# Performance work log

Hardware: AMD Instinct MI355X
Metric: run time of the kernel (lower is better)

Reference implementation:

```python
import jax, jax.numpy as jnp
import numpy as np

N, E, H, FN, FE = 50000, 800000, 128, 8, 4


def setup_inputs() -> dict:
    key = jax.random.key(0)
    ks = jax.random.split(key, 12)
    g = lambda k, shape: jax.random.normal(k, shape, dtype=jnp.float32) * 0.05
    return dict(
        x=jax.random.normal(ks[0], (N, FN), dtype=jnp.float32),
        edge_index=jax.random.randint(ks[1], (2, E), 0, N),
        edge_attr=jax.random.normal(ks[2], (E, FE), dtype=jnp.float32),
        W1=g(ks[3], (FN, H)), b1=jnp.zeros((H,), jnp.float32),
        W2=g(ks[4], (H, H)), b2=jnp.zeros((H,), jnp.float32),
        W3=g(ks[5], (H, H)), b3=jnp.zeros((H,), jnp.float32),
        We1=g(ks[6], (FE, H)), be1=jnp.zeros((H,), jnp.float32),
        We2=g(ks[7], (H, H)), be2=jnp.zeros((H,), jnp.float32),
        Wc1=g(ks[8], (3 * H, H)), bc1=jnp.zeros((H,), jnp.float32),
        Wc2=g(ks[9], (H, H // 2)), bc2=jnp.zeros((H // 2,), jnp.float32),
        Wc3=g(ks[10], (H // 2, 2)), bc3=jnp.zeros((2,), jnp.float32),
    )


def _gcn(h, W, b, row2, col2, norm, n):
    # GCNConv: transform, normalized message from source row2 -> target col2, scatter-add, bias
    h = h @ W
    msg = norm[:, None] * h[row2]  # [E+N, H]
    return jax.ops.segment_sum(msg, col2, num_segments=n) + b


def reference(x, edge_index, edge_attr, W1, b1, W2, b2, W3, b3,
              We1, be1, We2, be2, Wc1, bc1, Wc2, bc2, Wc3, bc3):
    n = x.shape[0]
    row, col = edge_index[0], edge_index[1]
    loop = jnp.arange(n)
    # add self-loops (PyG GCNConv default)
    row2 = jnp.concatenate([row, loop])
    col2 = jnp.concatenate([col, loop])
    deg = jax.ops.segment_sum(jnp.ones_like(col2, dtype=x.dtype), col2, num_segments=n)
    dinv = jnp.where(deg > 0, deg ** -0.5, 0.0)
    norm = dinv[row2] * dinv[col2]  # symmetric normalization per edge

    h = jax.nn.relu(_gcn(x, W1, b1, row2, col2, norm, n))
    h = jax.nn.relu(_gcn(h, W2, b2, row2, col2, norm, n))
    h = jax.nn.relu(_gcn(h, W3, b3, row2, col2, norm, n))

    # edge encoder MLP (dropout inactive in eval)
    ef = jax.nn.relu(edge_attr @ We1 + be1) @ We2 + be2

    # gather endpoint node features, concat with edge features
    ec = jnp.concatenate([h[row], h[col], ef], axis=1)  # [E, 3H]
    z = jax.nn.relu(ec @ Wc1 + bc1)
    z = jax.nn.relu(z @ Wc2 + bc2)
    logits = z @ Wc3 + bc3
    return jax.nn.log_softmax(logits, axis=1)
```

## Files before the change

### kernel.cpp

```cpp
#include <hip/hip_runtime.h>
#include <math.h>

#define H 128
#define STC 152
#define SOT 136
#define SPQ 136
#define Z2S 69

typedef __attribute__((ext_vector_type(8))) short short8;
typedef __attribute__((ext_vector_type(4))) float f32x4;

__device__ inline unsigned short f2bf(float f) {
    unsigned int u = __float_as_uint(f);
    return (unsigned short)((u + 0x7fffu + ((u >> 16) & 1u)) >> 16);
}
__device__ inline float bflo(unsigned int v) { return __uint_as_float(v << 16); }
__device__ inline float bfhi(unsigned int v) { return __uint_as_float(v & 0xffff0000u); }
__device__ inline float bf2f(unsigned short v) { return __uint_as_float(((unsigned int)v) << 16); }

__device__ inline void fma4(float4& acc, float a, const float4 w) {
    acc.x = fmaf(a, w.x, acc.x);
    acc.y = fmaf(a, w.y, acc.y);
    acc.z = fmaf(a, w.z, acc.z);
    acc.w = fmaf(a, w.w, acc.w);
}


__global__ void count_kernel(const int* __restrict__ col, int E, int* __restrict__ cnt) {
    int e = blockIdx.x * blockDim.x + threadIdx.x;
    if (e < E) atomicAdd(&cnt[col[e]], 1);
}

__global__ void scan_sum_kernel(const int* __restrict__ cnt, int N, int* __restrict__ bsum) {
    int b = blockIdx.x, t = threadIdx.x;
    int base = b * 1024 + t * 4;
    int s = 0;
#pragma unroll
    for (int g = 0; g < 4; ++g) {
        int i = base + g;
        if (i < N) s += cnt[i];
    }
    for (int off = 32; off >= 1; off >>= 1) s += __shfl_down(s, off, 64);
    __shared__ int ws[4];
    if ((t & 63) == 0) ws[t >> 6] = s;
    __syncthreads();
    if (t == 0) bsum[b] = ws[0] + ws[1] + ws[2] + ws[3];
}

__global__ void scan_offsets_kernel(const int* __restrict__ bsum, int nb,
                                    int* __restrict__ boff, int* __restrict__ col_start, int N) {
    int lane = threadIdx.x;
    int v = (lane < nb) ? bsum[lane] : 0;
    int incl = v;
    for (int off = 1; off < 64; off <<= 1) {
        int u = __shfl_up(incl, off, 64);
        if (lane >= off) incl += u;
    }
    if (lane < nb) boff[lane] = incl - v;
    if (lane == 63) col_start[N] = incl;
}

__global__ void scan_write_kernel(const int* __restrict__ cnt, int N, const int* __restrict__ boff,
                                  int* __restrict__ col_start, int* __restrict__ cursor,
                                  float* __restrict__ dinv) {
    int b = blockIdx.x, t = threadIdx.x;
    int lane = t & 63, wv = t >> 6;
    int base = b * 1024 + t * 4;
    int c[4];
    int s = 0;
#pragma unroll
    for (int g = 0; g < 4; ++g) {
        int i = base + g;
        c[g] = (i < N) ? cnt[i] : 0;
        s += c[g];
    }
    int incl = s;
    for (int off = 1; off < 64; off <<= 1) {
        int u = __shfl_up(incl, off, 64);
        if (lane >= off) incl += u;
    }
    __shared__ int ws[4];
    if (lane == 63) ws[wv] = incl;
    __syncthreads();
    int run = boff[b] + incl - s;
    for (int w = 0; w < wv; ++w) run += ws[w];
#pragma unroll
    for (int g = 0; g < 4; ++g) {
        int i = base + g;
        if (i < N) {
            col_start[i] = run;
            cursor[i] = run;
            dinv[i] = rsqrtf((float)(c[g] + 1));
            run += c[g];
        }
    }
}

__global__ void scatter_kernel(const int* __restrict__ row, const int* __restrict__ col, int E,
                               int* __restrict__ cursor, int* __restrict__ csc_src,
                               int2* __restrict__ csc_ec) {
    int e = blockIdx.x * blockDim.x + threadIdx.x;
    if (e < E) {
        int c = col[e];
        int p = atomicAdd(&cursor[c], 1);
        csc_src[p] = row[e];
        csc_ec[p] = make_int2(e, c);
    }
}


__global__ __launch_bounds__(256) void aggx_kernel(
    const float* __restrict__ x, const int* __restrict__ col_start,
    const int* __restrict__ csc_src, const float* __restrict__ dinv,
    float* __restrict__ aggx, int N) {
    int wv = threadIdx.x >> 6, lane = threadIdx.x & 63;
    int i = blockIdx.x * 4 + wv;
    if (i >= N) return;
    int f = lane & 7, j = lane >> 3;
    int s0 = col_start[i], s1 = col_start[i + 1];
    float acc = 0.f;
    int p = s0 + j;
    for (; p + 8 < s1; p += 16) {
        int sa = csc_src[p], sb = csc_src[p + 8];
        float va = dinv[sa] * x[sa * 8 + f];
        float vb = dinv[sb] * x[sb * 8 + f];
        acc += va + vb;
    }
    if (p < s1) {
        int s = csc_src[p];
        acc = fmaf(dinv[s], x[s * 8 + f], acc);
    }
    acc += __shfl_xor(acc, 8, 64);
    acc += __shfl_xor(acc, 16, 64);
    acc += __shfl_xor(acc, 32, 64);
    if (j == 0) {
        float di = dinv[i];
        aggx[i * 8 + f] = fmaf(di, acc, di * di * x[i * 8 + f]);
    }
}

__global__ void xform8bf_kernel(const float* __restrict__ aggx, const float* __restrict__ W,
                                const float* __restrict__ b, const float* __restrict__ dinv,
                                unsigned int* __restrict__ out, int N) {
    int t = blockIdx.x * 256 + threadIdx.x;
    int i = t >> 6, jp = t & 63;
    if (i >= N) return;
    const float* ar = aggx + i * 8;
    float sc = dinv[i];
    int j0 = jp * 2;
    float a0 = b[j0], a1 = b[j0 + 1];
#pragma unroll
    for (int k = 0; k < 8; ++k) {
        float av = ar[k];
        a0 = fmaf(av, W[k * 128 + j0], a0);
        a1 = fmaf(av, W[k * 128 + j0 + 1], a1);
    }
    out[(size_t)i * 64 + jp] = (unsigned int)f2bf(sc * fmaxf(a0, 0.f)) |
                               ((unsigned int)f2bf(sc * fmaxf(a1, 0.f)) << 16);
}

__global__ __launch_bounds__(256) void agg128bf_kernel(
    const unsigned int* __restrict__ hd, const int* __restrict__ col_start,
    const int* __restrict__ csc_src, const float* __restrict__ dinv,
    unsigned int* __restrict__ out, int N) {
    int wv = threadIdx.x >> 6, lane = threadIdx.x & 63;
    int i = blockIdx.x * 4 + wv;
    if (i >= N) return;
    int s0 = col_start[i], s1 = col_start[i + 1];
    float ax = 0.f, ay = 0.f;
    int p = s0;
    for (; p + 16 <= s1; p += 16) {
        unsigned int v[16];
#pragma unroll
        for (int k = 0; k < 16; ++k)
            v[k] = hd[(size_t)csc_src[p + k] * 64 + lane];
#pragma unroll
        for (int k = 0; k < 16; ++k) { ax += bflo(v[k]); ay += bfhi(v[k]); }
    }
    for (; p + 4 <= s1; p += 4) {
        unsigned int v0 = hd[(size_t)csc_src[p + 0] * 64 + lane];
        unsigned int v1 = hd[(size_t)csc_src[p + 1] * 64 + lane];
        unsigned int v2 = hd[(size_t)csc_src[p + 2] * 64 + lane];
        unsigned int v3 = hd[(size_t)csc_src[p + 3] * 64 + lane];
        ax += bflo(v0) + bflo(v1) + bflo(v2) + bflo(v3);
        ay += bfhi(v0) + bfhi(v1) + bfhi(v2) + bfhi(v3);
    }
    for (; p < s1; ++p) {
        unsigned int v = hd[(size_t)csc_src[p] * 64 + lane];
        ax += bflo(v); ay += bfhi(v);
    }
    float di = dinv[i];
    unsigned int vs = hd[(size_t)i * 64 + lane];
    float rx = di * (ax + bflo(vs));
    float ry = di * (ay + bfhi(vs));
    out[(size_t)i * 64 + lane] = (unsigned int)f2bf(rx) | ((unsigned int)f2bf(ry) << 16);
}

__global__ __launch_bounds__(256) void xform_mfma_kernel(
    const unsigned short* __restrict__ in, const unsigned short* __restrict__ Bp,
    const float* __restrict__ b, const float* __restrict__ scale,
    unsigned short* __restrict__ out, int N) {
    __shared__ __align__(16) unsigned short sm[64 * STC];
    int tid = threadIdx.x;
    int i0 = blockIdx.x * 64;
    for (int u = tid; u < 1024; u += 256) {
        int i = u >> 4, l = u & 15;
        int node = i0 + i; if (node >= N) node = N - 1;
        uint4 v = ((const uint4*)in)[(size_t)node * 16 + l];
        *(uint4*)&sm[i * STC + l * 8] = v;
    }
    __syncthreads();
    int lane = tid & 63, w = tid >> 6, lm = lane & 15, quad = lane >> 4;
    int nt0 = 2 * w, nt1 = 2 * w + 1;
    f32x4 acc0[4], acc1[4];
    {
        float bv0 = b[nt0 * 16 + lm], bv1 = b[nt1 * 16 + lm];
        for (int m = 0; m < 4; ++m)
            for (int r = 0; r < 4; ++r) { acc0[m][r] = bv0; acc1[m][r] = bv1; }
    }
#pragma unroll
    for (int s = 0; s < 4; ++s) {
        short8 b0 = *(const short8*)&Bp[((size_t)(s * 8 + nt0) * 64 + lane) * 8];
        short8 b1 = *(const short8*)&Bp[((size_t)(s * 8 + nt1) * 64 + lane) * 8];
#pragma unroll
        for (int m = 0; m < 4; ++m) {
            short8 afr = *(const short8*)&sm[(m * 16 + lm) * STC + s * 32 + quad * 8];
            acc0[m] = __builtin_amdgcn_mfma_f32_16x16x32_bf16(afr, b0, acc0[m], 0, 0, 0);
            acc1[m] = __builtin_amdgcn_mfma_f32_16x16x32_bf16(afr, b1, acc1[m], 0, 0, 0);
        }
    }
    __syncthreads();
    for (int m = 0; m < 4; ++m)
        for (int r = 0; r < 4; ++r) {
            int rw = m * 16 + quad * 4 + r;
            int node = i0 + rw; if (node >= N) node = N - 1;
            float sc = scale ? scale[node] : 1.f;
            sm[rw * SOT + nt0 * 16 + lm] = f2bf(sc * fmaxf(acc0[m][r], 0.f));
            sm[rw * SOT + nt1 * 16 + lm] = f2bf(sc * fmaxf(acc1[m][r], 0.f));
        }
    __syncthreads();
    for (int u = tid; u < 1024; u += 256) {
        int i = u >> 4, l = u & 15;
        int node = i0 + i;
        if (node < N)
            *(uint4*)&out[(size_t)node * 128 + l * 8] = *(uint4*)&sm[i * SOT + l * 8];
    }
}


__global__ void weff_kernel(const float* __restrict__ We2, const float* __restrict__ Wc1,
                            float* __restrict__ Weff) {
    int idx = blockIdx.x * blockDim.x + threadIdx.x;
    int k = idx >> 7, c = idx & 127;
    float acc = 0.f;
    for (int j = 0; j < 128; ++j)
        acc = fmaf(We2[k * 128 + j], Wc1[(256 + j) * 128 + c], acc);
    Weff[idx] = acc;
}

__global__ void bc1p_kernel(const float* __restrict__ bc1, const float* __restrict__ be2,
                            const float* __restrict__ Wc1, float* __restrict__ bc1p) {
    int c = threadIdx.x;
    float acc = bc1[c];
    for (int j = 0; j < 128; ++j)
        acc = fmaf(be2[j], Wc1[(256 + j) * 128 + c], acc);
    bc1p[c] = acc;
}

__global__ void packg_kernel(const float* __restrict__ src, unsigned short* __restrict__ dst) {
    int idx = blockIdx.x * 256 + threadIdx.x;
    int s = idx >> 9, nt = (idx >> 6) & 7, lane = idx & 63;
    int quad = lane >> 4, lm = lane & 15;
    int n = nt * 16 + lm, k0 = s * 32 + quad * 8;
    unsigned int p[4];
#pragma unroll
    for (int g = 0; g < 4; ++g) {
        p[g] = (unsigned int)f2bf(src[(k0 + 2 * g) * 128 + n]) |
               ((unsigned int)f2bf(src[(k0 + 2 * g + 1) * 128 + n]) << 16);
    }
    *(uint4*)&dst[(size_t)idx * 8] = make_uint4(p[0], p[1], p[2], p[3]);
}

__global__ void pack2_kernel(const float* __restrict__ Wc2, unsigned short* __restrict__ Bp2) {
    int idx = blockIdx.x * 256 + threadIdx.x;
    int s = idx >> 8, nt = (idx >> 6) & 3, lane = idx & 63;
    int quad = lane >> 4, lm = lane & 15;
    int n = nt * 16 + lm, k0 = s * 32 + quad * 8;
    unsigned int p[4];
#pragma unroll
    for (int g = 0; g < 4; ++g) {
        p[g] = (unsigned int)f2bf(Wc2[(k0 + 2 * g) * 64 + n]) |
               ((unsigned int)f2bf(Wc2[(k0 + 2 * g + 1) * 64 + n]) << 16);
    }
    *(uint4*)&Bp2[(size_t)idx * 8] = make_uint4(p[0], p[1], p[2], p[3]);
}

__global__ void packwe1_kernel(const float* __restrict__ We1, const float* __restrict__ be1,
                               unsigned short* __restrict__ BpE) {
    int idx = blockIdx.x * 256 + threadIdx.x;
    if (idx >= 512) return;
    int nt = idx >> 6, lane = idx & 63;
    int quad = lane >> 4, lm = lane & 15;
    int n = nt * 16 + lm, k0 = quad * 8;
    unsigned int p[4];
#pragma unroll
    for (int g = 0; g < 4; ++g) {
        int r0 = k0 + 2 * g, r1 = r0 + 1;
        float v0 = (r0 < 4) ? We1[r0 * 128 + n] : ((r0 == 4) ? be1[n] : 0.f);
        float v1 = (r1 < 4) ? We1[r1 * 128 + n] : ((r1 == 4) ? be1[n] : 0.f);
        p[g] = (unsigned int)f2bf(v0) | ((unsigned int)f2bf(v1) << 16);
    }
    *(uint4*)&BpE[(size_t)idx * 8] = make_uint4(p[0], p[1], p[2], p[3]);
}


__global__ __launch_bounds__(256) void h3pq_kernel(
    const unsigned short* __restrict__ in, const unsigned short* __restrict__ BpW3,
    const float* __restrict__ b3,
    const unsigned short* __restrict__ BpA, const unsigned short* __restrict__ BpB,
    const float* __restrict__ bc1p,
    unsigned short* __restrict__ P, unsigned short* __restrict__ Q, int N) {
    __shared__ __align__(16) unsigned short At[64 * STC];
    __shared__ __align__(16) unsigned short Hs[64 * SOT];
    int tid = threadIdx.x;
    int i0 = blockIdx.x * 64;
    for (int u = tid; u < 1024; u += 256) {
        int i = u >> 4, l = u & 15;
        int node = i0 + i; if (node >= N) node = N - 1;
        uint4 v = ((const uint4*)in)[(size_t)node * 16 + l];
        *(uint4*)&At[i * STC + l * 8] = v;
    }
    __syncthreads();
    int lane = tid & 63, w = tid >> 6, lm = lane & 15, quad = lane >> 4;

    {
        int nt0 = 2 * w, nt1 = 2 * w + 1;
        f32x4 a0[4], a1[4];
        float bv0 = b3[nt0 * 16 + lm], bv1 = b3[nt1 * 16 + lm];
        for (int m = 0; m < 4; ++m)
            for (int r = 0; r < 4; ++r) { a0[m][r] = bv0; a1[m][r] = bv1; }
#pragma unroll
        for (int s = 0; s < 4; ++s) {
            short8 b0 = *(const short8*)&BpW3[((size_t)(s * 8 + nt0) * 64 + lane) * 8];
            short8 b1 = *(const short8*)&BpW3[((size_t)(s * 8 + nt1) * 64 + lane) * 8];
#pragma unroll
            for (int m = 0; m < 4; ++m) {
                short8 afr = *(const short8*)&At[(m * 16 + lm) * STC + s * 32 + quad * 8];
                a0[m] = __builtin_amdgcn_mfma_f32_16x16x32_bf16(afr, b0, a0[m], 0, 0, 0);
                a1[m] = __builtin_amdgcn_mfma_f32_16x16x32_bf16(afr, b1, a1[m], 0, 0, 0);
            }
        }
        __syncthreads();
        for (int m = 0; m < 4; ++m)
            for (int r = 0; r < 4; ++r) {
                int rw = m * 16 + quad * 4 + r;
                Hs[rw * SOT + nt0 * 16 + lm] = f2bf(fmaxf(a0[m][r], 0.f));
                Hs[rw * SOT + nt1 * 16 + lm] = f2bf(fmaxf(a1[m][r], 0.f));
            }
    }
    __syncthreads();

    int half = w & 1;
    const unsigned short* Bp = (w >> 1) ? BpB : BpA;
    f32x4 acc[4][4];
    for (int nt = 0; nt < 4; ++nt) {
        float bv = (w >> 1) ? 0.f : bc1p[half * 64 + nt * 16 + lm];
        for (int m = 0; m < 4; ++m)
            for (int r = 0; r < 4; ++r) acc[nt][m][r] = bv;
    }
#pragma unroll
    for (int s = 0; s < 4; ++s) {
        short8 afr[4];
#pragma unroll
        for (int m = 0; m < 4; ++m)
            afr[m] = *(const short8*)&Hs[(m * 16 + lm) * SOT + s * 32 + quad * 8];
#pragma unroll
        for (int nt = 0; nt < 4; ++nt) {
            short8 bfr = *(const short8*)&Bp[((size_t)(s * 8 + half * 4 + nt) * 64 + lane) * 8];
#pragma unroll
            for (int m = 0; m < 4; ++m)
                acc[nt][m] = __builtin_amdgcn_mfma_f32_16x16x32_bf16(afr[m], bfr, acc[nt][m], 0, 0, 0);
        }
    }
    __syncthreads();
    unsigned short* St = At;

    if (w < 2) {
        for (int nt = 0; nt < 4; ++nt)
            for (int m = 0; m < 4; ++m)
                for (int r = 0; r < 4; ++r) {
                    int rw = m * 16 + quad * 4 + r;
                    St[rw * SOT + half * 64 + nt * 16 + lm] = f2bf(acc[nt][m][r]);
                }
    }
    __syncthreads();
    for (int u = tid; u < 1024; u += 256) {
        int i = u >> 4, l = u & 15;
        int node = i0 + i;
        if (node < N)
            *(uint4*)&P[(size_t)node * 128 + l * 8] = *(uint4*)&St[i * SOT + l * 8];
    }
    __syncthreads();
    if (w >= 2) {
        for (int nt = 0; nt < 4; ++nt)
            for (int m = 0; m < 4; ++m)
                for (int r = 0; r < 4; ++r) {
                    int rw = m * 16 + quad * 4 + r;
                    St[rw * SOT + half * 64 + nt * 16 + lm] = f2bf(acc[nt][m][r]);
                }
    }
    __syncthreads();
    for (int u = tid; u < 1024; u += 256) {
        int i = u >> 4, l = u & 15;
        int node = i0 + i;
        if (node < N)
            *(uint4*)&Q[(size_t)node * 128 + l * 8] = *(uint4*)&St[i * SOT + l * 8];
    }
}


__global__ __launch_bounds__(256, 4) void classifier_mfma2(
    const int* __restrict__ csc_src, const int2* __restrict__ csc_ec,
    const float* __restrict__ ea, const unsigned short* __restrict__ BpE,
    const unsigned short* __restrict__ P, const unsigned short* __restrict__ Q,
    const unsigned short* __restrict__ BpU, const unsigned short* __restrict__ Bp2,
    const float* __restrict__ bc2, const float* __restrict__ Wc3, const float* __restrict__ bc3,
    float* __restrict__ out, int E) {
    __shared__ __align__(16) unsigned char smem[37888];
    unsigned short* SpqB = (unsigned short*)smem;
    float* z2 = (float*)smem;
    unsigned short* At = (unsigned short*)(smem + 17664);
    unsigned short* z1 = At;
    float* part = (float*)(smem + 17664);
    int* sS = (int*)(smem + 37120);
    int* eS = sS + 64;
    int* cS = eS + 64;

    int tid = threadIdx.x;
    int lane = tid & 63, w = tid >> 6, lm = lane & 15, quad = lane >> 4;
    int e0 = blockIdx.x * 64;

    short8 bE0 = *(const short8*)&BpE[((size_t)(2 * w) * 64 + lane) * 8];
    short8 bE1 = *(const short8*)&BpE[((size_t)(2 * w + 1) * 64 + lane) * 8];
    short8 b0s[4], b1s[4], b2s[4];
#pragma unroll
    for (int s = 0; s < 4; ++s) {
        b0s[s] = *(const short8*)&BpU[((size_t)(s * 8 + 2 * w) * 64 + lane) * 8];
        b1s[s] = *(const short8*)&BpU[((size_t)(s * 8 + 2 * w + 1) * 64 + lane) * 8];
        b2s[s] = *(const short8*)&Bp2[((size_t)(s * 4 + w) * 64 + lane) * 8];
    }
    float bv2 = bc2[w * 16 + lm];

    if (tid < 64) {
        int p = e0 + tid; if (p >= E) p = E - 1;
        sS[tid] = csc_src[p];
        int2 ec = csc_ec[p];
        eS[tid] = ec.x; cS[tid] = ec.y;
    }
    __syncthreads();

    {
        const uint4* P4 = (const uint4*)P;
        const uint4* Q4 = (const uint4*)Q;
        int l = tid & 15;
#pragma unroll
        for (int j = 0; j < 4; ++j) {
            int i = (tid >> 4) + 16 * j;
            uint4 pv = P4[(size_t)sS[i] * 16 + l];
            uint4 qv = Q4[(size_t)cS[i] * 16 + l];
            unsigned int o0 = (unsigned int)f2bf(bflo(pv.x) + bflo(qv.x)) |
                              ((unsigned int)f2bf(bfhi(pv.x) + bfhi(qv.x)) << 16);
            unsigned int o1 = (unsigned int)f2bf(bflo(pv.y) + bflo(qv.y)) |
                              ((unsigned int)f2bf(bfhi(pv.y) + bfhi(qv.y)) << 16);
            unsigned int o2 = (unsigned int)f2bf(bflo(pv.z) + bflo(qv.z)) |
                              ((unsigned int)f2bf(bfhi(pv.z) + bfhi(qv.z)) << 16);
            unsigned int o3 = (unsigned int)f2bf(bflo(pv.w) + bflo(qv.w)) |
                              ((unsigned int)f2bf(bfhi(pv.w) + bfhi(qv.w)) << 16);
            *(uint4*)&SpqB[i * SPQ + l * 8] = make_uint4(o0, o1, o2, o3);
        }
    }

    short8 eaf[4];
#pragma unroll
    for (int m = 0; m < 4; ++m) eaf[m] = (short8){0, 0, 0, 0, 0, 0, 0, 0};
    if (quad == 0) {
#pragma unroll
        for (int m = 0; m < 4; ++m) {
            int ed = eS[m * 16 + lm];
            float4 a = ((const float4*)ea)[ed];
            eaf[m][0] = (short)f2bf(a.x);
            eaf[m][1] = (short)f2bf(a.y);
            eaf[m][2] = (short)f2bf(a.z);
            eaf[m][3] = (short)f2bf(a.w);
            eaf[m][4] = (short)0x3F80;
        }
    }

    {
        f32x4 zacc = {0.f, 0.f, 0.f, 0.f};
#pragma unroll
        for (int m = 0; m < 4; ++m) {
            f32x4 t0 = __builtin_amdgcn_mfma_f32_16x16x32_bf16(eaf[m], bE0, zacc, 0, 0, 0);
            f32x4 t1 = __builtin_amdgcn_mfma_f32_16x16x32_bf16(eaf[m], bE1, zacc, 0, 0, 0);
#pragma unroll
            for (int r = 0; r < 4; ++r) {
                int rw = m * 16 + quad * 4 + r;
                At[rw * STC + 32 * w + lm]      = f2bf(fmaxf(t0[r], 0.f));
                At[rw * STC + 32 * w + 16 + lm] = f2bf(fmaxf(t1[r], 0.f));
            }
        }
    }
    __syncthreads();

    f32x4 acc0[4], acc1[4];
    for (int m = 0; m < 4; ++m)
        for (int r = 0; r < 4; ++r) { acc0[m][r] = 0.f; acc1[m][r] = 0.f; }
#pragma unroll
    for (int s = 0; s < 4; ++s) {
#pragma unroll
        for (int m = 0; m < 4; ++m) {
            short8 afr = *(const short8*)&At[(m * 16 + lm) * STC + s * 32 + quad * 8];
            acc0[m] = __builtin_amdgcn_mfma_f32_16x16x32_bf16(afr, b0s[s], acc0[m], 0, 0, 0);
            acc1[m] = __builtin_amdgcn_mfma_f32_16x16x32_bf16(afr, b1s[s], acc1[m], 0, 0, 0);
        }
    }
    for (int m = 0; m < 4; ++m)
        for (int r = 0; r < 4; ++r) {
            int rw = m * 16 + quad * 4 + r;
            acc0[m][r] = fmaxf(acc0[m][r] + bf2f(SpqB[rw * SPQ + 32 * w + lm]), 0.f);
            acc1[m][r] = fmaxf(acc1[m][r] + bf2f(SpqB[rw * SPQ + 32 * w + 16 + lm]), 0.f);
        }
    __syncthreads();
    for (int m = 0; m < 4; ++m)
        for (int r = 0; r < 4; ++r) {
            int rw = m * 16 + quad * 4 + r;
            z1[rw * STC + 32 * w + lm]      = f2bf(acc0[m][r]);
            z1[rw * STC + 32 * w + 16 + lm] = f2bf(acc1[m][r]);
        }
    __syncthreads();

    {
        f32x4 acc2[4];
        for (int m = 0; m < 4; ++m)
            for (int r = 0; r < 4; ++r) acc2[m][r] = bv2;
#pragma unroll
        for (int s = 0; s < 4; ++s) {
#pragma unroll
            for (int m = 0; m < 4; ++m) {
                short8 afr = *(const short8*)&z1[(m * 16 + lm) * STC + s * 32 + quad * 8];
                acc2[m] = __builtin_amdgcn_mfma_f32_16x16x32_bf16(afr, b2s[s], acc2[m], 0, 0, 0);
            }
        }
        for (int m = 0; m < 4; ++m)
            for (int r = 0; r < 4; ++r)
                z2[(m * 16 + quad * 4 + r) * Z2S + w * 16 + lm] = fmaxf(acc2[m][r], 0.f);
    }
    __syncthreads();

    {
        int e = tid & 63, q = tid >> 6;
        int c = q & 1, hf = q >> 1;
        const float* zr = z2 + e * Z2S + hf * 32;
        const float* wc = Wc3 + hf * 64 + c;
        float acc = 0.f;
#pragma unroll 8
        for (int kk = 0; kk < 32; ++kk)
            acc = fmaf(zr[kk], wc[2 * kk], acc);
        part[q * 64 + e] = acc;
    }
    __syncthreads();
    if (tid < 64) {
        int p = e0 + tid;
        if (p < E) {
            float l0 = bc3[0] + part[tid] + part[128 + tid];
            float l1 = bc3[1] + part[64 + tid] + part[192 + tid];
            float m = fmaxf(l0, l1);
            float lse = m + logf(expf(l0 - m) + expf(l1 - m));
            ((float2*)out)[eS[tid]] = make_float2(l0 - lse, l1 - lse);
        }
    }
}


extern "C" void kernel_launch(void* const* d_in, const int* in_sizes, int n_in,
                              void* d_out, int out_size, void* d_ws, size_t ws_size,
                              hipStream_t stream) {
    const float* x   = (const float*)d_in[0];
    const int*   ei  = (const int*)d_in[1];
    const float* ea  = (const float*)d_in[2];
    const float* W1  = (const float*)d_in[3];
    const float* b1  = (const float*)d_in[4];
    const float* W2  = (const float*)d_in[5];
    const float* b2  = (const float*)d_in[6];
    const float* W3  = (const float*)d_in[7];
    const float* b3  = (const float*)d_in[8];
    const float* We1 = (const float*)d_in[9];
    const float* be1 = (const float*)d_in[10];
    const float* We2 = (const float*)d_in[11];
    const float* be2 = (const float*)d_in[12];
    const float* Wc1 = (const float*)d_in[13];
    const float* bc1 = (const float*)d_in[14];
    const float* Wc2 = (const float*)d_in[15];
    const float* bc2 = (const float*)d_in[16];
    const float* Wc3 = (const float*)d_in[17];
    const float* bc3 = (const float*)d_in[18];
    float* out = (float*)d_out;

    int N = in_sizes[0] / 8;
    int E = in_sizes[1] / 2;
    const int* row = ei;
    const int* col = ei + E;
    int NB = (N + 1023) / 1024;
    int ntiles = (E + 63) / 64;

    char* w = (char*)d_ws;
    auto alloc = [&](size_t bytes) { void* p = (void*)w; w += (bytes + 255) & ~(size_t)255; return p; };
    int*   cnt       = (int*)alloc((size_t)N * 4);
    int*   col_start = (int*)alloc((size_t)(N + 1) * 4);
    int*   cursor    = (int*)alloc((size_t)N * 4);
    int*   csc_src   = (int*)alloc((size_t)E * 4);
    int2*  csc_ec    = (int2*)alloc((size_t)E * 8);
    float* dinv      = (float*)alloc((size_t)N * 4);
    int*   bsum      = (int*)alloc(64 * 4);
    int*   boff      = (int*)alloc(64 * 4);
    float* Weff      = (float*)alloc(128 * 128 * 4);
    float* bc1p      = (float*)alloc(128 * 4);
    unsigned short* BpA  = (unsigned short*)alloc(32768);
    unsigned short* BpB  = (unsigned short*)alloc(32768);
    unsigned short* BpU  = (unsigned short*)alloc(32768);
    unsigned short* BpW2 = (unsigned short*)alloc(32768);
    unsigned short* BpW3 = (unsigned short*)alloc(32768);
    unsigned short* Bp2  = (unsigned short*)alloc(16384);
    unsigned short* BpE  = (unsigned short*)alloc(8192);
    float* aggx = (float*)alloc((size_t)N * 8 * 4);
    unsigned short* bufA = (unsigned short*)alloc((size_t)N * H * 2);
    unsigned short* bufB = (unsigned short*)alloc((size_t)N * H * 2);
    unsigned short* Pm   = (unsigned short*)alloc((size_t)N * H * 2);
    unsigned short* Qm   = (unsigned short*)alloc((size_t)N * H * 2);

    hipMemsetAsync(cnt, 0, (size_t)N * 4, stream);
    count_kernel<<<(E + 255) / 256, 256, 0, stream>>>(col, E, cnt);
    scan_sum_kernel<<<NB, 256, 0, stream>>>(cnt, N, bsum);
    scan_offsets_kernel<<<1, 64, 0, stream>>>(bsum, NB, boff, col_start, N);
    scan_write_kernel<<<NB, 256, 0, stream>>>(cnt, N, boff, col_start, cursor, dinv);
    scatter_kernel<<<(E + 255) / 256, 256, 0, stream>>>(row, col, E, cursor, csc_src, csc_ec);

    weff_kernel<<<64, 256, 0, stream>>>(We2, Wc1, Weff);
    bc1p_kernel<<<1, 128, 0, stream>>>(bc1, be2, Wc1, bc1p);
    packg_kernel<<<8, 256, 0, stream>>>(Wc1, BpA);
    packg_kernel<<<8, 256, 0, stream>>>(Wc1 + 128 * 128, BpB);
    packg_kernel<<<8, 256, 0, stream>>>(Weff, BpU);
    packg_kernel<<<8, 256, 0, stream>>>(W2, BpW2);
    packg_kernel<<<8, 256, 0, stream>>>(W3, BpW3);
    pack2_kernel<<<4, 256, 0, stream>>>(Wc2, Bp2);
    packwe1_kernel<<<2, 256, 0, stream>>>(We1, be1, BpE);

    aggx_kernel<<<(N + 3) / 4, 256, 0, stream>>>(x, col_start, csc_src, dinv, aggx, N);
    xform8bf_kernel<<<(N * 64 + 255) / 256, 256, 0, stream>>>(aggx, W1, b1, dinv,
                                                              (unsigned int*)bufA, N);
    agg128bf_kernel<<<(N + 3) / 4, 256, 0, stream>>>((const unsigned int*)bufA, col_start, csc_src,
                                                     dinv, (unsigned int*)bufB, N);
    xform_mfma_kernel<<<(N + 63) / 64, 256, 0, stream>>>(bufB, BpW2, b2, dinv, bufA, N);
    agg128bf_kernel<<<(N + 3) / 4, 256, 0, stream>>>((const unsigned int*)bufA, col_start, csc_src,
                                                     dinv, (unsigned int*)bufB, N);
    h3pq_kernel<<<(N + 63) / 64, 256, 0, stream>>>(bufB, BpW3, b3, BpA, BpB, bc1p, Pm, Qm, N);

    classifier_mfma2<<<ntiles, 256, 0, stream>>>(
        csc_src, csc_ec, ea, BpE, Pm, Qm, BpU, Bp2, bc2, Wc3, bc3, out, E);
}
```

Baseline: 462.4 us.

## Fuse GCN aggregation with per-layer transforms and merge weight-packing launches

```diff
diff --git a/kernel.cpp b/kernel.cpp
--- a/kernel.cpp
+++ b/kernel.cpp
@@ -109,145 +109,6 @@
 }
 
 
-__global__ __launch_bounds__(256) void aggx_kernel(
-    const float* __restrict__ x, const int* __restrict__ col_start,
-    const int* __restrict__ csc_src, const float* __restrict__ dinv,
-    float* __restrict__ aggx, int N) {
-    int wv = threadIdx.x >> 6, lane = threadIdx.x & 63;
-    int i = blockIdx.x * 4 + wv;
-    if (i >= N) return;
-    int f = lane & 7, j = lane >> 3;
-    int s0 = col_start[i], s1 = col_start[i + 1];
-    float acc = 0.f;
-    int p = s0 + j;
-    for (; p + 8 < s1; p += 16) {
-        int sa = csc_src[p], sb = csc_src[p + 8];
-        float va = dinv[sa] * x[sa * 8 + f];
-        float vb = dinv[sb] * x[sb * 8 + f];
-        acc += va + vb;
-    }
-    if (p < s1) {
-        int s = csc_src[p];
-        acc = fmaf(dinv[s], x[s * 8 + f], acc);
-    }
-    acc += __shfl_xor(acc, 8, 64);
-    acc += __shfl_xor(acc, 16, 64);
-    acc += __shfl_xor(acc, 32, 64);
-    if (j == 0) {
-        float di = dinv[i];
-        aggx[i * 8 + f] = fmaf(di, acc, di * di * x[i * 8 + f]);
-    }
-}
-
-__global__ void xform8bf_kernel(const float* __restrict__ aggx, const float* __restrict__ W,
-                                const float* __restrict__ b, const float* __restrict__ dinv,
-                                unsigned int* __restrict__ out, int N) {
-    int t = blockIdx.x * 256 + threadIdx.x;
-    int i = t >> 6, jp = t & 63;
-    if (i >= N) return;
-    const float* ar = aggx + i * 8;
-    float sc = dinv[i];
-    int j0 = jp * 2;
-    float a0 = b[j0], a1 = b[j0 + 1];
-#pragma unroll
-    for (int k = 0; k < 8; ++k) {
-        float av = ar[k];
-        a0 = fmaf(av, W[k * 128 + j0], a0);
-        a1 = fmaf(av, W[k * 128 + j0 + 1], a1);
-    }
-    out[(size_t)i * 64 + jp] = (unsigned int)f2bf(sc * fmaxf(a0, 0.f)) |
-                               ((unsigned int)f2bf(sc * fmaxf(a1, 0.f)) << 16);
-}
-
-__global__ __launch_bounds__(256) void agg128bf_kernel(
-    const unsigned int* __restrict__ hd, const int* __restrict__ col_start,
-    const int* __restrict__ csc_src, const float* __restrict__ dinv,
-    unsigned int* __restrict__ out, int N) {
-    int wv = threadIdx.x >> 6, lane = threadIdx.x & 63;
-    int i = blockIdx.x * 4 + wv;
-    if (i >= N) return;
-    int s0 = col_start[i], s1 = col_start[i + 1];
-    float ax = 0.f, ay = 0.f;
-    int p = s0;
-    for (; p + 16 <= s1; p += 16) {
-        unsigned int v[16];
-#pragma unroll
-        for (int k = 0; k < 16; ++k)
-            v[k] = hd[(size_t)csc_src[p + k] * 64 + lane];
-#pragma unroll
-        for (int k = 0; k < 16; ++k) { ax += bflo(v[k]); ay += bfhi(v[k]); }
-    }
-    for (; p + 4 <= s1; p += 4) {
-        unsigned int v0 = hd[(size_t)csc_src[p + 0] * 64 + lane];
-        unsigned int v1 = hd[(size_t)csc_src[p + 1] * 64 + lane];
-        unsigned int v2 = hd[(size_t)csc_src[p + 2] * 64 + lane];
-        unsigned int v3 = hd[(size_t)csc_src[p + 3] * 64 + lane];
-        ax += bflo(v0) + bflo(v1) + bflo(v2) + bflo(v3);
-        ay += bfhi(v0) + bfhi(v1) + bfhi(v2) + bfhi(v3);
-    }
-    for (; p < s1; ++p) {
-        unsigned int v = hd[(size_t)csc_src[p] * 64 + lane];
-        ax += bflo(v); ay += bfhi(v);
-    }
-    float di = dinv[i];
-    unsigned int vs = hd[(size_t)i * 64 + lane];
-    float rx = di * (ax + bflo(vs));
-    float ry = di * (ay + bfhi(vs));
-    out[(size_t)i * 64 + lane] = (unsigned int)f2bf(rx) | ((unsigned int)f2bf(ry) << 16);
-}
-
-__global__ __launch_bounds__(256) void xform_mfma_kernel(
-    const unsigned short* __restrict__ in, const unsigned short* __restrict__ Bp,
-    const float* __restrict__ b, const float* __restrict__ scale,
-    unsigned short* __restrict__ out, int N) {
-    __shared__ __align__(16) unsigned short sm[64 * STC];
-    int tid = threadIdx.x;
-    int i0 = blockIdx.x * 64;
-    for (int u = tid; u < 1024; u += 256) {
-        int i = u >> 4, l = u & 15;
-        int node = i0 + i; if (node >= N) node = N - 1;
-        uint4 v = ((const uint4*)in)[(size_t)node * 16 + l];
-        *(uint4*)&sm[i * STC + l * 8] = v;
-    }
-    __syncthreads();
-    int lane = tid & 63, w = tid >> 6, lm = lane & 15, quad = lane >> 4;
-    int nt0 = 2 * w, nt1 = 2 * w + 1;
-    f32x4 acc0[4], acc1[4];
-    {
-        float bv0 = b[nt0 * 16 + lm], bv1 = b[nt1 * 16 + lm];
-        for (int m = 0; m < 4; ++m)
-            for (int r = 0; r < 4; ++r) { acc0[m][r] = bv0; acc1[m][r] = bv1; }
-    }
-#pragma unroll
-    for (int s = 0; s < 4; ++s) {
-        short8 b0 = *(const short8*)&Bp[((size_t)(s * 8 + nt0) * 64 + lane) * 8];
-        short8 b1 = *(const short8*)&Bp[((size_t)(s * 8 + nt1) * 64 + lane) * 8];
-#pragma unroll
-        for (int m = 0; m < 4; ++m) {
-            short8 afr = *(const short8*)&sm[(m * 16 + lm) * STC + s * 32 + quad * 8];
-            acc0[m] = __builtin_amdgcn_mfma_f32_16x16x32_bf16(afr, b0, acc0[m], 0, 0, 0);
-            acc1[m] = __builtin_amdgcn_mfma_f32_16x16x32_bf16(afr, b1, acc1[m], 0, 0, 0);
-        }
-    }
-    __syncthreads();
-    for (int m = 0; m < 4; ++m)
-        for (int r = 0; r < 4; ++r) {
-            int rw = m * 16 + quad * 4 + r;
-            int node = i0 + rw; if (node >= N) node = N - 1;
-            float sc = scale ? scale[node] : 1.f;
-            sm[rw * SOT + nt0 * 16 + lm] = f2bf(sc * fmaxf(acc0[m][r], 0.f));
-            sm[rw * SOT + nt1 * 16 + lm] = f2bf(sc * fmaxf(acc1[m][r], 0.f));
-        }
-    __syncthreads();
-    for (int u = tid; u < 1024; u += 256) {
-        int i = u >> 4, l = u & 15;
-        int node = i0 + i;
-        if (node < N)
-            *(uint4*)&out[(size_t)node * 128 + l * 8] = *(uint4*)&sm[i * SOT + l * 8];
-    }
-}
-
-
 __global__ void weff_kernel(const float* __restrict__ We2, const float* __restrict__ Wc1,
                             float* __restrict__ Weff) {
     int idx = blockIdx.x * blockDim.x + threadIdx.x;
@@ -267,150 +128,320 @@
     bc1p[c] = acc;
 }
 
-__global__ void packg_kernel(const float* __restrict__ src, unsigned short* __restrict__ dst) {
-    int idx = blockIdx.x * 256 + threadIdx.x;
-    int s = idx >> 9, nt = (idx >> 6) & 7, lane = idx & 63;
-    int quad = lane >> 4, lm = lane & 15;
-    int n = nt * 16 + lm, k0 = s * 32 + quad * 8;
-    unsigned int p[4];
-#pragma unroll
-    for (int g = 0; g < 4; ++g) {
-        p[g] = (unsigned int)f2bf(src[(k0 + 2 * g) * 128 + n]) |
-               ((unsigned int)f2bf(src[(k0 + 2 * g + 1) * 128 + n]) << 16);
-    }
-    *(uint4*)&dst[(size_t)idx * 8] = make_uint4(p[0], p[1], p[2], p[3]);
-}
-
-__global__ void pack2_kernel(const float* __restrict__ Wc2, unsigned short* __restrict__ Bp2) {
-    int idx = blockIdx.x * 256 + threadIdx.x;
-    int s = idx >> 8, nt = (idx >> 6) & 3, lane = idx & 63;
-    int quad = lane >> 4, lm = lane & 15;
-    int n = nt * 16 + lm, k0 = s * 32 + quad * 8;
-    unsigned int p[4];
-#pragma unroll
-    for (int g = 0; g < 4; ++g) {
-        p[g] = (unsigned int)f2bf(Wc2[(k0 + 2 * g) * 64 + n]) |
-               ((unsigned int)f2bf(Wc2[(k0 + 2 * g + 1) * 64 + n]) << 16);
-    }
-    *(uint4*)&Bp2[(size_t)idx * 8] = make_uint4(p[0], p[1], p[2], p[3]);
-}
-
-__global__ void packwe1_kernel(const float* __restrict__ We1, const float* __restrict__ be1,
-                               unsigned short* __restrict__ BpE) {
-    int idx = blockIdx.x * 256 + threadIdx.x;
-    if (idx >= 512) return;
-    int nt = idx >> 6, lane = idx & 63;
-    int quad = lane >> 4, lm = lane & 15;
-    int n = nt * 16 + lm, k0 = quad * 8;
-    unsigned int p[4];
-#pragma unroll
-    for (int g = 0; g < 4; ++g) {
-        int r0 = k0 + 2 * g, r1 = r0 + 1;
-        float v0 = (r0 < 4) ? We1[r0 * 128 + n] : ((r0 == 4) ? be1[n] : 0.f);
-        float v1 = (r1 < 4) ? We1[r1 * 128 + n] : ((r1 == 4) ? be1[n] : 0.f);
-        p[g] = (unsigned int)f2bf(v0) | ((unsigned int)f2bf(v1) << 16);
-    }
-    *(uint4*)&BpE[(size_t)idx * 8] = make_uint4(p[0], p[1], p[2], p[3]);
-}
-
-
-__global__ __launch_bounds__(256) void h3pq_kernel(
-    const unsigned short* __restrict__ in, const unsigned short* __restrict__ BpW3,
-    const float* __restrict__ b3,
+__global__ void pack_all_kernel(const float* __restrict__ Wc1, const float* __restrict__ Weff,
+                                const float* __restrict__ W2, const float* __restrict__ W3,
+                                const float* __restrict__ Wc2,
+                                const float* __restrict__ We1, const float* __restrict__ be1,
+                                unsigned short* __restrict__ BpA, unsigned short* __restrict__ BpB,
+                                unsigned short* __restrict__ BpU, unsigned short* __restrict__ BpW2,
+                                unsigned short* __restrict__ BpW3, unsigned short* __restrict__ Bp2,
+                                unsigned short* __restrict__ BpE) {
+    int b = blockIdx.x;
+    if (b < 40) {
+        const float* src;
+        unsigned short* dst;
+        int which = b >> 3;
+        if (which == 0)      { src = Wc1;          dst = BpA; }
+        else if (which == 1) { src = Wc1 + 16384;  dst = BpB; }
+        else if (which == 2) { src = Weff;         dst = BpU; }
+        else if (which == 3) { src = W2;           dst = BpW2; }
+        else                 { src = W3;           dst = BpW3; }
+        int idx = (b & 7) * 256 + threadIdx.x;
+        int s = idx >> 9, nt = (idx >> 6) & 7, lane = idx & 63;
+        int quad = lane >> 4, lm = lane & 15;
+        int n = nt * 16 + lm, k0 = s * 32 + quad * 8;
+        unsigned int p[4];
+#pragma unroll
+        for (int g = 0; g < 4; ++g) {
+            p[g] = (unsigned int)f2bf(src[(k0 + 2 * g) * 128 + n]) |
+                   ((unsigned int)f2bf(src[(k0 + 2 * g + 1) * 128 + n]) << 16);
+        }
+        *(uint4*)&dst[(size_t)idx * 8] = make_uint4(p[0], p[1], p[2], p[3]);
+    } else if (b < 44) {
+        int idx = (b - 40) * 256 + threadIdx.x;
+        int s = idx >> 8, nt = (idx >> 6) & 3, lane = idx & 63;
+        int quad = lane >> 4, lm = lane & 15;
+        int n = nt * 16 + lm, k0 = s * 32 + quad * 8;
+        unsigned int p[4];
+#pragma unroll
+        for (int g = 0; g < 4; ++g) {
+            p[g] = (unsigned int)f2bf(Wc2[(k0 + 2 * g) * 64 + n]) |
+                   ((unsigned int)f2bf(Wc2[(k0 + 2 * g + 1) * 64 + n]) << 16);
+        }
+        *(uint4*)&Bp2[(size_t)idx * 8] = make_uint4(p[0], p[1], p[2], p[3]);
+    } else {
+        int idx = (b - 44) * 256 + threadIdx.x;
+        if (idx < 512) {
+            int nt = idx >> 6, lane = idx & 63;
+            int quad = lane >> 4, lm = lane & 15;
+            int n = nt * 16 + lm, k0 = quad * 8;
+            unsigned int p[4];
+#pragma unroll
+            for (int g = 0; g < 4; ++g) {
+                int r0 = k0 + 2 * g, r1 = r0 + 1;
+                float v0 = (r0 < 4) ? We1[r0 * 128 + n] : ((r0 == 4) ? be1[n] : 0.f);
+                float v1 = (r1 < 4) ? We1[r1 * 128 + n] : ((r1 == 4) ? be1[n] : 0.f);
+                p[g] = (unsigned int)f2bf(v0) | ((unsigned int)f2bf(v1) << 16);
+            }
+            *(uint4*)&BpE[(size_t)idx * 8] = make_uint4(p[0], p[1], p[2], p[3]);
+        }
+    }
+}
+
+
+__global__ __launch_bounds__(256) void layer1_kernel(
+    const float* __restrict__ x, const int* __restrict__ col_start,
+    const int* __restrict__ csc_src, const float* __restrict__ dinv,
+    const float* __restrict__ W1, const float* __restrict__ b1,
+    unsigned int* __restrict__ out, int N) {
+    __shared__ float ax_s[64][8];
+    int tid = threadIdx.x, wv = tid >> 6, lane = tid & 63;
+    int i0 = blockIdx.x * 64;
+    int f = lane & 7, j = lane >> 3;
+    for (int k = 0; k < 16; ++k) {
+        int i = i0 + wv * 16 + k;
+        if (i < N) {
+            int s0 = col_start[i], s1 = col_start[i + 1];
+            float acc = 0.f;
+            int p = s0 + j;
+            for (; p + 8 < s1; p += 16) {
+                int sa = csc_src[p], sb = csc_src[p + 8];
+                acc += dinv[sa] * x[sa * 8 + f] + dinv[sb] * x[sb * 8 + f];
+            }
+            if (p < s1) {
+                int s = csc_src[p];
+                acc = fmaf(dinv[s], x[s * 8 + f], acc);
+            }
+            acc += __shfl_xor(acc, 8, 64);
+            acc += __shfl_xor(acc, 16, 64);
+            acc += __shfl_xor(acc, 32, 64);
+            if (j == 0) {
+                float di = dinv[i];
+                ax_s[wv * 16 + k][f] = fmaf(di, acc, di * di * x[i * 8 + f]);
+            }
+        }
+    }
+    __syncthreads();
+    for (int u = tid; u < 4096; u += 256) {
+        int k = u >> 6, jp = u & 63;
+        int node = i0 + k;
+        if (node >= N) continue;
+        const float* ar = ax_s[k];
+        float sc = dinv[node];
+        int j0 = jp * 2;
+        float a0 = b1[j0], a1 = b1[j0 + 1];
+#pragma unroll
+        for (int kk = 0; kk < 8; ++kk) {
+            float av = ar[kk];
+            a0 = fmaf(av, W1[kk * 128 + j0], a0);
+            a1 = fmaf(av, W1[kk * 128 + j0 + 1], a1);
+        }
+        out[(size_t)node * 64 + jp] = (unsigned int)f2bf(sc * fmaxf(a0, 0.f)) |
+                                      ((unsigned int)f2bf(sc * fmaxf(a1, 0.f)) << 16);
+    }
+}
+
+__global__ __launch_bounds__(512) void layer2_kernel(
+    const unsigned int* __restrict__ hd, const int* __restrict__ col_start,
+    const int* __restrict__ csc_src, const float* __restrict__ dinv,
+    const unsigned short* __restrict__ Bp, const float* __restrict__ b,
+    const float* __restrict__ scale, unsigned short* __restrict__ out, int N) {
+    __shared__ __align__(16) unsigned short At[64 * STC];
+    int tid = threadIdx.x, wv = tid >> 6, lane = tid & 63;
+    int lm = lane & 15, quad = lane >> 4;
+    int i0 = blockIdx.x * 64;
+
+    short8 bs[4];
+#pragma unroll
+    for (int s = 0; s < 4; ++s)
+        bs[s] = *(const short8*)&Bp[((size_t)(s * 8 + wv) * 64 + lane) * 8];
+    float bv = b[wv * 16 + lm];
+
+    unsigned int* At32 = (unsigned int*)At;
+    for (int k = 0; k < 8; ++k) {
+        int i = i0 + wv * 8 + k;
+        int ii = (i < N) ? i : N - 1;
+        int s0 = col_start[ii], s1 = col_start[ii + 1];
+        float ax = 0.f, ay = 0.f;
+        int p = s0;
+        for (; p + 16 <= s1; p += 16) {
+            unsigned int v[16];
+#pragma unroll
+            for (int t = 0; t < 16; ++t) v[t] = hd[(size_t)csc_src[p + t] * 64 + lane];
+#pragma unroll
+            for (int t = 0; t < 16; ++t) { ax += bflo(v[t]); ay += bfhi(v[t]); }
+        }
+        for (; p + 4 <= s1; p += 4) {
+            unsigned int v0 = hd[(size_t)csc_src[p + 0] * 64 + lane];
+            unsigned int v1 = hd[(size_t)csc_src[p + 1] * 64 + lane];
+            unsigned int v2 = hd[(size_t)csc_src[p + 2] * 64 + lane];
+            unsigned int v3 = hd[(size_t)csc_src[p + 3] * 64 + lane];
+            ax += bflo(v0) + bflo(v1) + bflo(v2) + bflo(v3);
+            ay += bfhi(v0) + bfhi(v1) + bfhi(v2) + bfhi(v3);
+        }
+        for (; p < s1; ++p) {
+            unsigned int v = hd[(size_t)csc_src[p] * 64 + lane];
+            ax += bflo(v); ay += bfhi(v);
+        }
+        float di = dinv[ii];
+        unsigned int vs = hd[(size_t)ii * 64 + lane];
+        float rx = di * (ax + bflo(vs));
+        float ry = di * (ay + bfhi(vs));
+        At32[(wv * 8 + k) * 76 + lane] = (unsigned int)f2bf(rx) | ((unsigned int)f2bf(ry) << 16);
+    }
+    __syncthreads();
+
+    f32x4 acc[4];
+    for (int m = 0; m < 4; ++m)
+        for (int r = 0; r < 4; ++r) acc[m][r] = bv;
+#pragma unroll
+    for (int s = 0; s < 4; ++s) {
+#pragma unroll
+        for (int m = 0; m < 4; ++m) {
+            short8 afr = *(const short8*)&At[(m * 16 + lm) * STC + s * 32 + quad * 8];
+            acc[m] = __builtin_amdgcn_mfma_f32_16x16x32_bf16(afr, bs[s], acc[m], 0, 0, 0);
+        }
+    }
+    __syncthreads();
+    for (int m = 0; m < 4; ++m)
+        for (int r = 0; r < 4; ++r) {
+            int rw = m * 16 + quad * 4 + r;
+            int node = i0 + rw; if (node >= N) node = N - 1;
+            float sc = scale ? scale[node] : 1.f;
+            At[rw * SOT + wv * 16 + lm] = f2bf(sc * fmaxf(acc[m][r], 0.f));
+        }
+    __syncthreads();
+    for (int u = tid; u < 1024; u += 512) {
+        int i = u >> 4, l = u & 15;
+        int node = i0 + i;
+        if (node < N)
+            *(uint4*)&out[(size_t)node * 128 + l * 8] = *(uint4*)&At[i * SOT + l * 8];
+    }
+}
+
+__global__ __launch_bounds__(512) void layer3_kernel(
+    const unsigned int* __restrict__ hd, const int* __restrict__ col_start,
+    const int* __restrict__ csc_src, const float* __restrict__ dinv,
+    const unsigned short* __restrict__ BpW3, const float* __restrict__ b3,
     const unsigned short* __restrict__ BpA, const unsigned short* __restrict__ BpB,
     const float* __restrict__ bc1p,
     unsigned short* __restrict__ P, unsigned short* __restrict__ Q, int N) {
     __shared__ __align__(16) unsigned short At[64 * STC];
     __shared__ __align__(16) unsigned short Hs[64 * SOT];
-    int tid = threadIdx.x;
+    int tid = threadIdx.x, wv = tid >> 6, lane = tid & 63;
+    int lm = lane & 15, quad = lane >> 4;
     int i0 = blockIdx.x * 64;
-    for (int u = tid; u < 1024; u += 256) {
-        int i = u >> 4, l = u & 15;
-        int node = i0 + i; if (node >= N) node = N - 1;
-        uint4 v = ((const uint4*)in)[(size_t)node * 16 + l];
-        *(uint4*)&At[i * STC + l * 8] = v;
-    }
-    __syncthreads();
-    int lane = tid & 63, w = tid >> 6, lm = lane & 15, quad = lane >> 4;
+
+    short8 bw3[4];
+#pragma unroll
+    for (int s = 0; s < 4; ++s)
+        bw3[s] = *(const short8*)&BpW3[((size_t)(s * 8 + wv) * 64 + lane) * 8];
+    float bv3 = b3[wv * 16 + lm];
+
+    unsigned int* At32 = (unsigned int*)At;
+    for (int k = 0; k < 8; ++k) {
+        int i = i0 + wv * 8 + k;
+        int ii = (i < N) ? i : N - 1;
+        int s0 = col_start[ii], s1 = col_start[ii + 1];
+        float ax = 0.f, ay = 0.f;
+        int p = s0;
+        for (; p + 16 <= s1; p += 16) {
+            unsigned int v[16];
+#pragma unroll
+            for (int t = 0; t < 16; ++t) v[t] = hd[(size_t)csc_src[p + t] * 64 + lane];
+#pragma unroll
+            for (int t = 0; t < 16; ++t) { ax += bflo(v[t]); ay += bfhi(v[t]); }
+        }
+        for (; p + 4 <= s1; p += 4) {
+            unsigned int v0 = hd[(size_t)csc_src[p + 0] * 64 + lane];
+            unsigned int v1 = hd[(size_t)csc_src[p + 1] * 64 + lane];
+            unsigned int v2 = hd[(size_t)csc_src[p + 2] * 64 + lane];
+            unsigned int v3 = hd[(size_t)csc_src[p + 3] * 64 + lane];
+            ax += bflo(v0) + bflo(v1) + bflo(v2) + bflo(v3);
+            ay += bfhi(v0) + bfhi(v1) + bfhi(v2) + bfhi(v3);
+        }
+        for (; p < s1; ++p) {
+            unsigned int v = hd[(size_t)csc_src[p] * 64 + lane];
+            ax += bflo(v); ay += bfhi(v);
+        }
+        float di = dinv[ii];
+        unsigned int vs = hd[(size_t)ii * 64 + lane];
+        float rx = di * (ax + bflo(vs));
+        float ry = di * (ay + bfhi(vs));
+        At32[(wv * 8 + k) * 76 + lane] = (unsigned int)f2bf(rx) | ((unsigned int)f2bf(ry) << 16);
+    }
+    __syncthreads();
 
     {
-        int nt0 = 2 * w, nt1 = 2 * w + 1;
-        f32x4 a0[4], a1[4];
-        float bv0 = b3[nt0 * 16 + lm], bv1 = b3[nt1 * 16 + lm];
+        f32x4 acc[4];
         for (int m = 0; m < 4; ++m)
-            for (int r = 0; r < 4; ++r) { a0[m][r] = bv0; a1[m][r] = bv1; }
+            for (int r = 0; r < 4; ++r) acc[m][r] = bv3;
 #pragma unroll
         for (int s = 0; s < 4; ++s) {
-            short8 b0 = *(const short8*)&BpW3[((size_t)(s * 8 + nt0) * 64 + lane) * 8];
-            short8 b1 = *(const short8*)&BpW3[((size_t)(s * 8 + nt1) * 64 + lane) * 8];
 #pragma unroll
             for (int m = 0; m < 4; ++m) {
                 short8 afr = *(const short8*)&At[(m * 16 + lm) * STC + s * 32 + quad * 8];
-                a0[m] = __builtin_amdgcn_mfma_f32_16x16x32_bf16(afr, b0, a0[m], 0, 0, 0);
-                a1[m] = __builtin_amdgcn_mfma_f32_16x16x32_bf16(afr, b1, a1[m], 0, 0, 0);
-            }
-        }
-        __syncthreads();
+                acc[m] = __builtin_amdgcn_mfma_f32_16x16x32_bf16(afr, bw3[s], acc[m], 0, 0, 0);
+            }
+        }
         for (int m = 0; m < 4; ++m)
             for (int r = 0; r < 4; ++r) {
                 int rw = m * 16 + quad * 4 + r;
-                Hs[rw * SOT + nt0 * 16 + lm] = f2bf(fmaxf(a0[m][r], 0.f));
-                Hs[rw * SOT + nt1 * 16 + lm] = f2bf(fmaxf(a1[m][r], 0.f));
-            }
-    }
-    __syncthreads();
-
-    int half = w & 1;
-    const unsigned short* Bp = (w >> 1) ? BpB : BpA;
-    f32x4 acc[4][4];
-    for (int nt = 0; nt < 4; ++nt) {
-        float bv = (w >> 1) ? 0.f : bc1p[half * 64 + nt * 16 + lm];
+                Hs[rw * SOT + wv * 16 + lm] = f2bf(fmaxf(acc[m][r], 0.f));
+            }
+    }
+    __syncthreads();
+
+    int sel = wv >> 2, g = wv & 3;
+    int nt0 = 2 * g, nt1 = 2 * g + 1;
+    const unsigned short* Bp = sel ? BpB : BpA;
+    f32x4 a0[4], a1[4];
+    {
+        float bv0 = sel ? 0.f : bc1p[nt0 * 16 + lm];
+        float bv1 = sel ? 0.f : bc1p[nt1 * 16 + lm];
         for (int m = 0; m < 4; ++m)
-            for (int r = 0; r < 4; ++r) acc[nt][m][r] = bv;
+            for (int r = 0; r < 4; ++r) { a0[m][r] = bv0; a1[m][r] = bv1; }
     }
 #pragma unroll
     for (int s = 0; s < 4; ++s) {
-        short8 afr[4];
-#pragma unroll
+        short8 b0 = *(const short8*)&Bp[((size_t)(s * 8 + nt0) * 64 + lane) * 8];
+        short8 b1 = *(const short8*)&Bp[((size_t)(s * 8 + nt1) * 64 + lane) * 8];
+#pragma unroll
+        for (int m = 0; m < 4; ++m) {
+            short8 afr = *(const short8*)&Hs[(m * 16 + lm) * SOT + s * 32 + quad * 8];
+            a0[m] = __builtin_amdgcn_mfma_f32_16x16x32_bf16(afr, b0, a0[m], 0, 0, 0);
+            a1[m] = __builtin_amdgcn_mfma_f32_16x16x32_bf16(afr, b1, a1[m], 0, 0, 0);
+        }
+    }
+    __syncthreads();
+    unsigned short* St = At;
+
+    if (sel == 0) {
         for (int m = 0; m < 4; ++m)
-            afr[m] = *(const short8*)&Hs[(m * 16 + lm) * SOT + s * 32 + quad * 8];
-#pragma unroll
-        for (int nt = 0; nt < 4; ++nt) {
-            short8 bfr = *(const short8*)&Bp[((size_t)(s * 8 + half * 4 + nt) * 64 + lane) * 8];
-#pragma unroll
-            for (int m = 0; m < 4; ++m)
-                acc[nt][m] = __builtin_amdgcn_mfma_f32_16x16x32_bf16(afr[m], bfr, acc[nt][m], 0, 0, 0);
-        }
-    }
-    __syncthreads();
-    unsigned short* St = At;
-
-    if (w < 2) {
-        for (int nt = 0; nt < 4; ++nt)
-            for (int m = 0; m < 4; ++m)
-                for (int r = 0; r < 4; ++r) {
-                    int rw = m * 16 + quad * 4 + r;
-                    St[rw * SOT + half * 64 + nt * 16 + lm] = f2bf(acc[nt][m][r]);
-                }
-    }
-    __syncthreads();
-    for (int u = tid; u < 1024; u += 256) {
+            for (int r = 0; r < 4; ++r) {
+                int rw = m * 16 + quad * 4 + r;
+                St[rw * SOT + nt0 * 16 + lm] = f2bf(a0[m][r]);
+                St[rw * SOT + nt1 * 16 + lm] = f2bf(a1[m][r]);
+            }
+    }
+    __syncthreads();
+    for (int u = tid; u < 1024; u += 512) {
         int i = u >> 4, l = u & 15;
         int node = i0 + i;
         if (node < N)
             *(uint4*)&P[(size_t)node * 128 + l * 8] = *(uint4*)&St[i * SOT + l * 8];
     }
     __syncthreads();
-    if (w >= 2) {
-        for (int nt = 0; nt < 4; ++nt)
-            for (int m = 0; m < 4; ++m)
-                for (int r = 0; r < 4; ++r) {
-                    int rw = m * 16 + quad * 4 + r;
-                    St[rw * SOT + half * 64 + nt * 16 + lm] = f2bf(acc[nt][m][r]);
-                }
-    }
-    __syncthreads();
-    for (int u = tid; u < 1024; u += 256) {
+    if (sel == 1) {
+        for (int m = 0; m < 4; ++m)
+            for (int r = 0; r < 4; ++r) {
+                int rw = m * 16 + quad * 4 + r;
+                St[rw * SOT + nt0 * 16 + lm] = f2bf(a0[m][r]);
+                St[rw * SOT + nt1 * 16 + lm] = f2bf(a1[m][r]);
+            }
+    }
+    __syncthreads();
+    for (int u = tid; u < 1024; u += 512) {
         int i = u >> 4, l = u & 15;
         int node = i0 + i;
         if (node < N)
@@ -612,6 +643,7 @@
     const int* col = ei + E;
     int NB = (N + 1023) / 1024;
     int ntiles = (E + 63) / 64;
+    int nodetiles = (N + 63) / 64;
 
     char* w = (char*)d_ws;
     auto alloc = [&](size_t bytes) { void* p = (void*)w; w += (bytes + 255) & ~(size_t)255; return p; };
@@ -632,7 +664,6 @@
     unsigned short* BpW3 = (unsigned short*)alloc(32768);
     unsigned short* Bp2  = (unsigned short*)alloc(16384);
     unsigned short* BpE  = (unsigned short*)alloc(8192);
-    float* aggx = (float*)alloc((size_t)N * 8 * 4);
     unsigned short* bufA = (unsigned short*)alloc((size_t)N * H * 2);
     unsigned short* bufB = (unsigned short*)alloc((size_t)N * H * 2);
     unsigned short* Pm   = (unsigned short*)alloc((size_t)N * H * 2);
@@ -647,23 +678,15 @@
 
     weff_kernel<<<64, 256, 0, stream>>>(We2, Wc1, Weff);
     bc1p_kernel<<<1, 128, 0, stream>>>(bc1, be2, Wc1, bc1p);
-    packg_kernel<<<8, 256, 0, stream>>>(Wc1, BpA);
-    packg_kernel<<<8, 256, 0, stream>>>(Wc1 + 128 * 128, BpB);
-    packg_kernel<<<8, 256, 0, stream>>>(Weff, BpU);
-    packg_kernel<<<8, 256, 0, stream>>>(W2, BpW2);
-    packg_kernel<<<8, 256, 0, stream>>>(W3, BpW3);
-    pack2_kernel<<<4, 256, 0, stream>>>(Wc2, Bp2);
-    packwe1_kernel<<<2, 256, 0, stream>>>(We1, be1, BpE);
-
-    aggx_kernel<<<(N + 3) / 4, 256, 0, stream>>>(x, col_start, csc_src, dinv, aggx, N);
-    xform8bf_kernel<<<(N * 64 + 255) / 256, 256, 0, stream>>>(aggx, W1, b1, dinv,
-                                                              (unsigned int*)bufA, N);
-    agg128bf_kernel<<<(N + 3) / 4, 256, 0, stream>>>((const unsigned int*)bufA, col_start, csc_src,
-                                                     dinv, (unsigned int*)bufB, N);
-    xform_mfma_kernel<<<(N + 63) / 64, 256, 0, stream>>>(bufB, BpW2, b2, dinv, bufA, N);
-    agg128bf_kernel<<<(N + 3) / 4, 256, 0, stream>>>((const unsigned int*)bufA, col_start, csc_src,
-                                                     dinv, (unsigned int*)bufB, N);
-    h3pq_kernel<<<(N + 63) / 64, 256, 0, stream>>>(bufB, BpW3, b3, BpA, BpB, bc1p, Pm, Qm, N);
+    pack_all_kernel<<<46, 256, 0, stream>>>(Wc1, Weff, W2, W3, Wc2, We1, be1,
+                                            BpA, BpB, BpU, BpW2, BpW3, Bp2, BpE);
+
+    layer1_kernel<<<nodetiles, 256, 0, stream>>>(x, col_start, csc_src, dinv, W1, b1,
+                                                 (unsigned int*)bufA, N);
+    layer2_kernel<<<nodetiles, 512, 0, stream>>>((const unsigned int*)bufA, col_start, csc_src,
+                                                 dinv, BpW2, b2, dinv, bufB, N);
+    layer3_kernel<<<nodetiles, 512, 0, stream>>>((const unsigned int*)bufB, col_start, csc_src,
+                                                 dinv, BpW3, b3, BpA, BpB, bc1p, Pm, Qm, N);
 
     classifier_mfma2<<<ntiles, 256, 0, stream>>>(
         csc_src, csc_ec, ea, BpE, Pm, Qm, BpU, Bp2, bc2, Wc3, bc3, out, E);
```

Measured after the change: 501.7 us. 1.08x slower.
